# Kernel tuning notes

Hardware: AMD Instinct MI355X
Metric: run time of the kernel (lower is better)

The kernel has to match this reference:

```python
import jax, jax.numpy as jnp
import numpy as np

RADIUS = 0.3
NSAMPLE = 16
NPOINT = 256
EPS = 1e-5


def setup_inputs() -> dict:
    key = jax.random.key(0)
    ks = jax.random.split(key, 12)
    B, N, C = 16, 16384, 288
    d = {
        "xyz": jax.random.uniform(ks[0], (B, N, 3), jnp.float32),
        "features": jax.random.normal(ks[1], (B, C, N), jnp.float32),
    }
    cin = [C + 3, C, C]  # use_xyz adds 3 to first SharedMLP width
    for i in range(3):
        d[f"W{i}"] = jax.random.normal(ks[2 + i], (C, cin[i]), jnp.float32) / np.float32(np.sqrt(cin[i]))
        d[f"g{i}"] = jnp.ones((C,), jnp.float32)
        d[f"b{i}"] = jnp.zeros((C,), jnp.float32)
        d[f"m{i}"] = jax.random.normal(ks[5 + i], (C,), jnp.float32) * 0.1
        d[f"v{i}"] = jax.random.uniform(ks[8 + i], (C,), jnp.float32, minval=0.5, maxval=1.5)
    return d


def fps(xyz, npoint):
    """Farthest point sampling. xyz: (B,N,3) -> inds (B,npoint) int32."""
    B, N, _ = xyz.shape
    d0 = jnp.full((B, N), 1e10, xyz.dtype)
    i0 = jnp.zeros((B,), jnp.int32)  # CUDA kernel starts from index 0

    def step(carry, _):
        dist, idx = carry
        cur = jnp.take_along_axis(xyz, idx[:, None, None], axis=1)  # (B,1,3)
        d = jnp.sum((xyz - cur) ** 2, axis=-1)  # (B,N)
        dist = jnp.minimum(dist, d)
        nxt = jnp.argmax(dist, axis=-1).astype(jnp.int32)
        return (dist, nxt), idx

    _, inds = jax.lax.scan(step, (d0, i0), None, length=npoint)
    return inds.T  # (B, npoint)


def ball_query(xyz, new_xyz):
    """xyz: (B,N,3), new_xyz: (B,S,3) -> idx (B,S,NSAMPLE) int32.
    First NSAMPLE in-radius indices; pad with the first found index (CUDA semantics)."""
    N = xyz.shape[1]
    d2 = jnp.sum((new_xyz[:, :, None, :] - xyz[:, None, :, :]) ** 2, axis=-1)  # (B,S,N)
    mask = d2 < RADIUS * RADIUS
    cand = jnp.where(mask, jnp.arange(N, dtype=jnp.int32), jnp.int32(N))
    cand = jnp.sort(cand, axis=-1)[..., :NSAMPLE]
    first = cand[..., :1]
    return jnp.where(cand == N, first, cand)


def _mlp_bn_relu(h, W, g, b, m, v):
    # 1x1 Conv2d (no bias) + BatchNorm (running stats) + ReLU on (B,C,S,K)
    h = jnp.einsum('oc,bcsk->bosk', W, h)
    scale = (g * jax.lax.rsqrt(v + EPS))[:, None, None]
    return jax.nn.relu((h - m[:, None, None]) * scale + b[:, None, None])


def reference(xyz, features, W0, g0, b0, m0, v0, W1, g1, b1, m1, v1, W2, g2, b2, m2, v2):
    inds = fps(xyz, NPOINT)                                   # (B,S)
    new_xyz = jax.vmap(lambda p, i: p[i])(xyz, inds)          # (B,S,3)
    idx = ball_query(xyz, new_xyz)                            # (B,S,K)
    g_xyz = jax.vmap(lambda p, i: p[i])(xyz, idx)             # (B,S,K,3)
    g_xyz = (g_xyz - new_xyz[:, :, None, :]) / RADIUS         # normalize_xyz
    g_feat = jax.vmap(lambda f, i: f[:, i])(features, idx)    # (B,C,S,K)
    h = jnp.concatenate([jnp.transpose(g_xyz, (0, 3, 1, 2)), g_feat], axis=1)  # (B,C+3,S,K)
    for (W, g, b, m, v) in ((W0, g0, b0, m0, v0), (W1, g1, b1, m1, v1), (W2, g2, b2, m2, v2)):
        h = _mlp_bn_relu(h, W, g, b, m, v)
    new_features = jnp.max(h, axis=-1)                        # (B,C,S) max-pool over nsample
    return new_xyz, new_features, inds
```

## Files before the change

kernel.cpp:

```cpp
#include <hip/hip_runtime.h>
#include <hip/hip_bf16.h>
#include <string.h>

#define NPT   16384
#define NBAT  16
#define CH    288
#define SP    256
#define KS    16
#define OFF_FEAT 12288L
#define OFF_IND  1191936L

__device__ __forceinline__ float bfbits(unsigned short u){
  unsigned int x = ((unsigned int)u) << 16; float f; __builtin_memcpy(&f,&x,4); return f;
}
__device__ __forceinline__ float ldf(const void* p, long i, int isb){
  if (isb) return __bfloat162float(((const __hip_bfloat16*)p)[i]);
  return ((const float*)p)[i];
}
__device__ __forceinline__ void sto(void* p, long i, float v, int isb){
  if (isb) ((__hip_bfloat16*)p)[i] = __float2bfloat16(v);
  else     ((float*)p)[i] = v;
}
__device__ __forceinline__ void gload_lds(const void* g, void* l){
  __builtin_amdgcn_global_load_lds((const __attribute__((address_space(1))) void*)g,
      (__attribute__((address_space(3))) void*)l, 16, 0, 0);
}

typedef __attribute__((ext_vector_type(8))) short bf16x8;
typedef __attribute__((ext_vector_type(4))) float f32x4;

__global__ void detect_k(const void* __restrict__ xyz, int* __restrict__ flag){
  __shared__ float red[256];
  const int t = threadIdx.x;
  const unsigned short* u = (const unsigned short*)xyz;
  float m = 0.f;
  for (int i = t; i < 4096; i += 256){
    float f = fabsf(bfbits(u[i]));
    if (f != f) f = 1e30f;
    m = fmaxf(m, f);
  }
  red[t] = m; __syncthreads();
  for (int s = 128; s; s >>= 1){ if (t < s) red[t] = fmaxf(red[t], red[t+s]); __syncthreads(); }
  if (t == 0) *flag = (red[0] < 2.0f) ? 1 : 0;
}

__global__ __launch_bounds__(256) void cvtxyz_k(const void* __restrict__ xyz,
    const int* __restrict__ flag, float* __restrict__ X, float* __restrict__ Y,
    float* __restrict__ Z){
  const int e = blockIdx.x*256 + threadIdx.x;
  const int isb = *flag;
  float v = ldf(xyz, e, isb);
  int b = e / (NPT*3), r = e - b*(NPT*3), i = r/3, c = r - i*3;
  float* P = (c==0) ? X : ((c==1) ? Y : Z);
  P[b*NPT + i] = v;
}

__global__ __launch_bounds__(256) void cvtw_k(const void* __restrict__ W,
    const void* __restrict__ g, const void* __restrict__ bb,
    const void* __restrict__ m, const void* __restrict__ v,
    const int* __restrict__ flag, __hip_bfloat16* __restrict__ Wbf,
    float* __restrict__ scale, float* __restrict__ shift, int Kin){
  const int isb = *flag;
  const int idx = blockIdx.x*256 + threadIdx.x;
  if (idx < 288*296){
    int o = idx / 296, k = idx - o*296;
    float val = (k < Kin) ? ldf(W, (long)o*Kin + k, isb) : 0.f;
    Wbf[idx] = __float2bfloat16(val);
  }
  if (idx < 288){
    float sc = ldf(g, idx, isb) * rsqrtf(ldf(v, idx, isb) + 1e-5f);
    scale[idx] = sc;
    shift[idx] = ldf(bb, idx, isb) - ldf(m, idx, isb)*sc;
  }
}

__global__ __launch_bounds__(1024) __attribute__((amdgpu_waves_per_eu(4,4)))
void fps_k(const float* __restrict__ X,
    const float* __restrict__ Y, const float* __restrict__ Z,
    const int* __restrict__ flag, float* __restrict__ nxyz, void* __restrict__ dout){
  #pragma clang fp contract(off)
  const int b = blockIdx.x, t = threadIdx.x;
  const int base = b*NPT;
  float px[16], py[16], pz[16], dist[16];
  #pragma unroll
  for (int i=0;i<16;i++){
    px[i] = X[base + t + i*1024];
    py[i] = Y[base + t + i*1024];
    pz[i] = Z[base + t + i*1024];
    dist[i] = 1e10f;
  }
  __shared__ unsigned long long rk[2][16];
  __shared__ float ox[SP], oy[SP], oz[SP];
  __shared__ int   oi[SP];
  const int lane = t & 63, wid = t >> 6;
  const unsigned int lbase = 16383u - (unsigned int)t;
  float cx = X[base], cy = Y[base], cz = Z[base];
  int cur = 0;
  for (int it=0; it<SP; it++){
    if (t == 0){ ox[it]=cx; oy[it]=cy; oz[it]=cz; oi[it]=cur; }
    unsigned long long best = 0ull;
    #pragma unroll
    for (int i=0;i<16;i++){
      float dx = px[i]-cx, dy = py[i]-cy, dz = pz[i]-cz;
      float d2 = dx*dx + dy*dy; d2 = d2 + dz*dz;
      float dn = fminf(dist[i], d2); dist[i] = dn;
      unsigned long long key = ((unsigned long long)__float_as_uint(dn) << 32)
                             | (unsigned long long)(lbase - (unsigned int)(i*1024));
      best = (key > best) ? key : best;
    }
    #pragma unroll
    for (int off=32; off; off>>=1){
      unsigned long long o = __shfl_down(best, off, 64);
      best = (o > best) ? o : best;
    }
    const int p = it & 1;
    if (lane == 0) rk[p][wid] = best;
    __syncthreads();
    unsigned long long g0 = rk[p][0], g1 = rk[p][1], g2 = rk[p][2], g3 = rk[p][3];
    #pragma unroll
    for (int w=4; w<16; w+=4){
      unsigned long long a0=rk[p][w], a1=rk[p][w+1], a2=rk[p][w+2], a3=rk[p][w+3];
      g0=(a0>g0)?a0:g0; g1=(a1>g1)?a1:g1; g2=(a2>g2)?a2:g2; g3=(a3>g3)?a3:g3;
    }
    g0=(g1>g0)?g1:g0; g2=(g3>g2)?g3:g2; g0=(g2>g0)?g2:g0;
    cur = 16383 - (int)(unsigned int)g0;
    cx = X[base+cur]; cy = Y[base+cur]; cz = Z[base+cur];
  }
  __syncthreads();
  if (t < SP){
    const int isb = *flag;
    const long bs = (long)b*SP + t;
    float fx=ox[t], fy=oy[t], fz=oz[t]; int ii=oi[t];
    nxyz[bs*3+0]=fx; nxyz[bs*3+1]=fy; nxyz[bs*3+2]=fz;
    sto(dout, bs*3+0, fx, isb);
    sto(dout, bs*3+1, fy, isb);
    sto(dout, bs*3+2, fz, isb);
    sto(dout, OFF_IND + bs, (float)ii, isb);
  }
}

__global__ __launch_bounds__(256) void ballq_k(const float* __restrict__ X,
    const float* __restrict__ Y, const float* __restrict__ Z,
    const float* __restrict__ nxyz, int* __restrict__ bidx){
  #pragma clang fp contract(off)
  const int gw = (blockIdx.x*256 + threadIdx.x) >> 6;
  const int lane = threadIdx.x & 63;
  const int b = gw >> 8, base = b*NPT;
  const float cx = nxyz[gw*3+0], cy = nxyz[gw*3+1], cz = nxyz[gw*3+2];
  int cnt = 0, first = 0; bool havef = false;
  for (int st = 0; st < NPT && cnt < KS; st += 64){
    const int id = st + lane;
    float dx = X[base+id]-cx, dy = Y[base+id]-cy, dz = Z[base+id]-cz;
    float d2 = dx*dx + dy*dy; d2 = d2 + dz*dz;
    unsigned long long mk = __ballot(d2 <= 0.09f);
    if (mk){
      if (!havef){ first = st + __builtin_ctzll(mk); havef = true; }
      int rank = cnt + __popcll(mk & ((1ull<<lane)-1ull));
      if (((mk>>lane)&1ull) && rank < KS) bidx[gw*KS + rank] = id;
      cnt += __popcll(mk);
    }
  }
  if (cnt < KS && lane >= cnt && lane < KS) bidx[gw*KS + lane] = first;
}

__global__ __launch_bounds__(256) void gather_k(const void* __restrict__ xyz,
    const void* __restrict__ feat, const int* __restrict__ flag,
    const int* __restrict__ bidx, const float* __restrict__ nxyz,
    __hip_bfloat16* __restrict__ h0){
  __shared__ __hip_bfloat16 tile[64*296];
  const int isb = *flag;
  const int t = threadIdx.x, n0 = blockIdx.x*64;
  const int nl = t >> 2, cg = t & 3;
  const int n = n0 + nl, b = n >> 12, s = n >> 4;
  const int id = bidx[n];
  for (int j=0; j<74; j++){
    int c = cg*74 + j;
    float vv = 0.f;
    if (c < 3)       vv = (ldf(xyz, ((long)b*NPT + id)*3 + c, isb) - nxyz[(long)s*3 + c]) / 0.3f;
    else if (c < 291) vv = ldf(feat, ((long)b*CH + (c-3))*(long)NPT + id, isb);
    tile[nl*296 + c] = __float2bfloat16(vv);
  }
  __syncthreads();
  const uint4* src = (const uint4*)tile;
  uint4* dst = (uint4*)((char*)h0 + (long)n0*592);
  for (int j = t; j < 2368; j += 256) dst[j] = src[j];
}

__global__ __launch_bounds__(256, 2) void gemm_k(
    const __hip_bfloat16* __restrict__ A, int astr,
    const __hip_bfloat16* __restrict__ W,
    const float* __restrict__ scale, const float* __restrict__ shift,
    __hip_bfloat16* __restrict__ Out, int ostr,
    int ktiles, int kvalid){
  extern __shared__ char lds[];
  const int t = threadIdx.x, lane = t & 63, wid = t >> 6;
  const int wm = wid & 1, wo = wid >> 1;
  const int bx = blockIdx.x, by = blockIdx.y;
  {
    const char* src = (const char*)(A + (long)bx*128*astr);
    const int chunks = (128*astr*2) >> 10;
    for (int c = wid; c < chunks; c += 4)
      gload_lds(src + c*1024 + lane*16, lds + c*1024);
  }
  f32x4 acc[4][3];
  #pragma unroll
  for (int mf=0; mf<4; mf++)
    #pragma unroll
    for (int of=0; of<3; of++) acc[mf][of] = (f32x4){0.f,0.f,0.f,0.f};

  const int mrow  = wm*64 + (lane & 15);
  const int kg    = (lane >> 4) * 8;
  const int obase = by*96 + wo*48 + (lane & 15);
  __syncthreads();

  for (int kt = 0; kt < ktiles; kt++){
    const int k0 = kt*32 + kg;
    const bool z = (k0 >= kvalid);
    const int k0c = z ? 0 : k0;
    bf16x8 a[4], bf[3];
    #pragma unroll
    for (int mf=0; mf<4; mf++)
      a[mf] = *(const bf16x8*)(lds + ((long)(mrow + mf*16)*astr + k0c)*2);
    if (z){
      bf16x8 zz = {0,0,0,0,0,0,0,0};
      #pragma unroll
      for (int mf=0; mf<4; mf++) a[mf] = zz;
    }
    #pragma unroll
    for (int of=0; of<3; of++)
      bf[of] = *(const bf16x8*)(W + (long)(obase + of*16)*296 + k0c);
    #pragma unroll
    for (int mf=0; mf<4; mf++)
      #pragma unroll
      for (int of=0; of<3; of++)
        acc[mf][of] = __builtin_amdgcn_mfma_f32_16x16x32_bf16(a[mf], bf[of], acc[mf][of], 0, 0, 0);
  }

  float sc[3], sh[3];
  #pragma unroll
  for (int of=0; of<3; of++){ sc[of] = scale[obase + of*16]; sh[of] = shift[obase + of*16]; }
  #pragma unroll
  for (int mf=0; mf<4; mf++)
    #pragma unroll
    for (int of=0; of<3; of++)
      #pragma unroll
      for (int r=0; r<4; r++){
        const long row = (long)bx*128 + wm*64 + mf*16 + (lane>>4)*4 + r;
        const int o = obase + of*16;
        float vv = acc[mf][of][r]*sc[of] + sh[of];
        Out[row*ostr + o] = __float2bfloat16(fmaxf(vv, 0.f));
      }
}

__global__ __launch_bounds__(256) void maxk_k(const __hip_bfloat16* __restrict__ h,
    const int* __restrict__ flag, void* __restrict__ dout){
  __shared__ __hip_bfloat16 tile[128*288];
  const int isb = *flag;
  const int t = threadIdx.x;
  const int b = blockIdx.x >> 5, s0 = (blockIdx.x & 31)*8;
  const long n0 = (long)b*4096 + (long)s0*16;
  {
    const char* src = (const char*)(h + n0*288);
    for (int c = (t>>6); c < 72; c += 4)
      gload_lds(src + c*1024 + (t&63)*16, (char*)tile + c*1024);
  }
  __syncthreads();
  for (int o = t; o < 288; o += 256){
    float mx[8];
    #pragma unroll
    for (int sl=0; sl<8; sl++){
      float m = -1e30f;
      #pragma unroll
      for (int kk=0; kk<16; kk++)
        m = fmaxf(m, __bfloat162float(tile[(sl*16 + kk)*288 + o]));
      mx[sl] = m;
    }
    const long e0 = OFF_FEAT + (long)b*73728 + (long)o*256 + s0;
    if (isb){
      unsigned short u[8];
      #pragma unroll
      for (int sl=0; sl<8; sl++){
        __hip_bfloat16 hb = __float2bfloat16(mx[sl]);
        __builtin_memcpy(&u[sl], &hb, 2);
      }
      uint4 pk; __builtin_memcpy(&pk, u, 16);
      *(uint4*)((__hip_bfloat16*)dout + e0) = pk;
    } else {
      float* fo = (float*)dout + e0;
      *(float4*)fo     = make_float4(mx[0],mx[1],mx[2],mx[3]);
      *(float4*)(fo+4) = make_float4(mx[4],mx[5],mx[6],mx[7]);
    }
  }
}

extern "C" void kernel_launch(void* const* d_in, const int* in_sizes, int n_in,
                              void* d_out, int out_size, void* d_ws, size_t ws_size,
                              hipStream_t stream){
  const void* xyz  = d_in[0];
  const void* feat = d_in[1];
  const void* W0 = d_in[2];  const void* g0 = d_in[3];  const void* b0 = d_in[4];
  const void* m0 = d_in[5];  const void* v0 = d_in[6];
  const void* W1 = d_in[7];  const void* g1 = d_in[8];  const void* b1 = d_in[9];
  const void* m1 = d_in[10]; const void* v1 = d_in[11];
  const void* W2 = d_in[12]; const void* g2 = d_in[13]; const void* b2 = d_in[14];
  const void* m2 = d_in[15]; const void* v2 = d_in[16];

  char* ws = (char*)d_ws;
  int*   flag  = (int*)ws;
  float* sc0   = (float*)(ws + 64);
  float* sh0   = sc0 + 288;
  float* sc1   = sc0 + 576;  float* sh1 = sc0 + 864;
  float* sc2   = sc0 + 1152; float* sh2 = sc0 + 1440;
  __hip_bfloat16* Wb0 = (__hip_bfloat16*)(ws + 7040);
  __hip_bfloat16* Wb1 = Wb0 + 288*296;
  __hip_bfloat16* Wb2 = Wb1 + 288*296;
  float* nxyz = (float*)(ws + 518656);
  int*   bidx = (int*)(ws + 567808);
  float* X    = (float*)(ws + 1048576);
  float* Y    = X + NBAT*NPT;
  float* Z    = Y + NBAT*NPT;
  __hip_bfloat16* bufA = (__hip_bfloat16*)(ws + 1048576);
  __hip_bfloat16* bufB = (__hip_bfloat16*)(ws + 1048576 + 38797312);

  detect_k<<<1, 256, 0, stream>>>(xyz, flag);
  cvtxyz_k<<<3072, 256, 0, stream>>>(xyz, flag, X, Y, Z);
  cvtw_k<<<333, 256, 0, stream>>>(W0, g0, b0, m0, v0, flag, Wb0, sc0, sh0, 291);
  cvtw_k<<<333, 256, 0, stream>>>(W1, g1, b1, m1, v1, flag, Wb1, sc1, sh1, 288);
  cvtw_k<<<333, 256, 0, stream>>>(W2, g2, b2, m2, v2, flag, Wb2, sc2, sh2, 288);
  fps_k<<<NBAT, 1024, 0, stream>>>(X, Y, Z, flag, nxyz, d_out);
  ballq_k<<<1024, 256, 0, stream>>>(X, Y, Z, nxyz, bidx);
  gather_k<<<1024, 256, 0, stream>>>(xyz, feat, flag, bidx, nxyz, bufA);
  gemm_k<<<dim3(512,3), 256, 128*296*2, stream>>>(bufA, 296, Wb0, sc0, sh0, bufB, 288, 10, 296);
  gemm_k<<<dim3(512,3), 256, 128*288*2, stream>>>(bufB, 288, Wb1, sc1, sh1, bufA, 296, 9, 288);
  gemm_k<<<dim3(512,3), 256, 128*296*2, stream>>>(bufA, 296, Wb2, sc2, sh2, bufB, 288, 9, 288);
  maxk_k<<<512, 256, 0, stream>>>(bufB, flag, d_out);
}
```

Before: 1.061 ms.

## Morton-sort points per batch and skip FPS updates via per-wave bounding boxes

A new kernel bins each batch's points into a 16^3 Morton grid and counting-sorts them, keeping the original indices, so every wavefront in FPS owns a spatially compact cluster. FPS computes per-wave bounding boxes and skips the distance update and key reduction when the box's lower-bound distance to the new centroid exceeds the wave's current max min-distance. The final reduction uses shuffles and readfirstlane. This adds a sort pass and reuses the bufB workspace before the GEMMs; ties and near-equal cases depend on the 0.9999 safety margin.

```diff
diff --git a/kernel.cpp b/kernel.cpp
--- a/kernel.cpp
+++ b/kernel.cpp
@@ -24,6 +24,9 @@
 __device__ __forceinline__ void gload_lds(const void* g, void* l){
   __builtin_amdgcn_global_load_lds((const __attribute__((address_space(1))) void*)g,
       (__attribute__((address_space(3))) void*)l, 16, 0, 0);
+}
+__device__ __forceinline__ unsigned spread4(unsigned x){
+  return (x&1u) | ((x&2u)<<2) | ((x&4u)<<4) | ((x&8u)<<6);
 }
 
 typedef __attribute__((ext_vector_type(8))) short bf16x8;
@@ -74,56 +77,132 @@
   }
 }
 
+__global__ __launch_bounds__(1024) void sort_k(const float* __restrict__ X,
+    const float* __restrict__ Y, const float* __restrict__ Z,
+    float* __restrict__ X2, float* __restrict__ Y2, float* __restrict__ Z2,
+    int* __restrict__ I2){
+  __shared__ int hist[4096];
+  __shared__ int wtot[16];
+  const int b = blockIdx.x, t = threadIdx.x, base = b*NPT;
+  for (int j = t; j < 4096; j += 1024) hist[j] = 0;
+  __syncthreads();
+  int cell[16]; float lx[16], ly[16], lz[16];
+  #pragma unroll
+  for (int i=0;i<16;i++){
+    const int id = t + i*1024;
+    float x = X[base+id], y = Y[base+id], z = Z[base+id];
+    lx[i]=x; ly[i]=y; lz[i]=z;
+    int cx = (int)(x*16.f); cx = cx<0?0:(cx>15?15:cx);
+    int cy = (int)(y*16.f); cy = cy<0?0:(cy>15?15:cy);
+    int cz = (int)(z*16.f); cz = cz<0?0:(cz>15?15:cz);
+    cell[i] = (int)(spread4((unsigned)cx) | (spread4((unsigned)cy)<<1) | (spread4((unsigned)cz)<<2));
+    atomicAdd(&hist[cell[i]], 1);
+  }
+  __syncthreads();
+  int s0 = hist[t*4], s1 = hist[t*4+1], s2 = hist[t*4+2], s3 = hist[t*4+3];
+  int ls = s0+s1+s2+s3;
+  int sc = ls;
+  #pragma unroll
+  for (int off=1; off<64; off<<=1){
+    int o = __shfl_up(sc, off, 64);
+    if ((t&63) >= off) sc += o;
+  }
+  if ((t&63) == 63) wtot[t>>6] = sc;
+  __syncthreads();
+  int wpre = 0;
+  #pragma unroll
+  for (int w=0; w<16; w++) wpre += (w < (t>>6)) ? wtot[w] : 0;
+  const int ebase = wpre + sc - ls;
+  hist[t*4]   = ebase;
+  hist[t*4+1] = ebase + s0;
+  hist[t*4+2] = ebase + s0 + s1;
+  hist[t*4+3] = ebase + s0 + s1 + s2;
+  __syncthreads();
+  #pragma unroll
+  for (int i=0;i<16;i++){
+    const int dst = atomicAdd(&hist[cell[i]], 1);
+    X2[base+dst] = lx[i]; Y2[base+dst] = ly[i]; Z2[base+dst] = lz[i];
+    I2[base+dst] = t + i*1024;
+  }
+}
+
 __global__ __launch_bounds__(1024) __attribute__((amdgpu_waves_per_eu(4,4)))
-void fps_k(const float* __restrict__ X,
-    const float* __restrict__ Y, const float* __restrict__ Z,
+void fps_k(const float* __restrict__ X, const float* __restrict__ Y,
+    const float* __restrict__ Z,
+    const float* __restrict__ X2, const float* __restrict__ Y2,
+    const float* __restrict__ Z2, const int* __restrict__ I2,
     const int* __restrict__ flag, float* __restrict__ nxyz, void* __restrict__ dout){
   #pragma clang fp contract(off)
   const int b = blockIdx.x, t = threadIdx.x;
   const int base = b*NPT;
+  const int lane = t & 63, wid = t >> 6;
   float px[16], py[16], pz[16], dist[16];
+  unsigned int li[16];
+  const int p0 = base + wid*1024 + lane;
   #pragma unroll
   for (int i=0;i<16;i++){
-    px[i] = X[base + t + i*1024];
-    py[i] = Y[base + t + i*1024];
-    pz[i] = Z[base + t + i*1024];
+    px[i] = X2[p0 + i*64];
+    py[i] = Y2[p0 + i*64];
+    pz[i] = Z2[p0 + i*64];
+    li[i] = 16383u - (unsigned)I2[p0 + i*64];
     dist[i] = 1e10f;
   }
-  __shared__ unsigned long long rk[2][16];
+  float bxn=px[0],bxx=px[0],byn=py[0],byx=py[0],bzn=pz[0],bzx=pz[0];
+  #pragma unroll
+  for (int i=1;i<16;i++){
+    bxn=fminf(bxn,px[i]); bxx=fmaxf(bxx,px[i]);
+    byn=fminf(byn,py[i]); byx=fmaxf(byx,py[i]);
+    bzn=fminf(bzn,pz[i]); bzx=fmaxf(bzx,pz[i]);
+  }
+  #pragma unroll
+  for (int off=32; off; off>>=1){
+    bxn=fminf(bxn,__shfl_xor(bxn,off,64)); bxx=fmaxf(bxx,__shfl_xor(bxx,off,64));
+    byn=fminf(byn,__shfl_xor(byn,off,64)); byx=fmaxf(byx,__shfl_xor(byx,off,64));
+    bzn=fminf(bzn,__shfl_xor(bzn,off,64)); bzx=fmaxf(bzx,__shfl_xor(bzx,off,64));
+  }
+  __shared__ unsigned long long slot[2][16];
   __shared__ float ox[SP], oy[SP], oz[SP];
   __shared__ int   oi[SP];
-  const int lane = t & 63, wid = t >> 6;
-  const unsigned int lbase = 16383u - (unsigned int)t;
   float cx = X[base], cy = Y[base], cz = Z[base];
   int cur = 0;
+  unsigned long long wkey = 0ull;
+  float wavemax = 1e30f;
   for (int it=0; it<SP; it++){
     if (t == 0){ ox[it]=cx; oy[it]=cy; oz[it]=cz; oi[it]=cur; }
-    unsigned long long best = 0ull;
-    #pragma unroll
-    for (int i=0;i<16;i++){
-      float dx = px[i]-cx, dy = py[i]-cy, dz = pz[i]-cz;
-      float d2 = dx*dx + dy*dy; d2 = d2 + dz*dz;
-      float dn = fminf(dist[i], d2); dist[i] = dn;
-      unsigned long long key = ((unsigned long long)__float_as_uint(dn) << 32)
-                             | (unsigned long long)(lbase - (unsigned int)(i*1024));
-      best = (key > best) ? key : best;
-    }
-    #pragma unroll
-    for (int off=32; off; off>>=1){
-      unsigned long long o = __shfl_down(best, off, 64);
-      best = (o > best) ? o : best;
+    float ddx = fmaxf(fmaxf(bxn-cx, cx-bxx), 0.f);
+    float ddy = fmaxf(fmaxf(byn-cy, cy-byx), 0.f);
+    float ddz = fmaxf(fmaxf(bzn-cz, cz-bzx), 0.f);
+    float lb = ddx*ddx + ddy*ddy + ddz*ddz;
+    if (!(lb * 0.9999f > wavemax)){
+      unsigned long long best = 0ull;
+      #pragma unroll
+      for (int i=0;i<16;i++){
+        float dx = px[i]-cx, dy = py[i]-cy, dz = pz[i]-cz;
+        float d2 = dx*dx + dy*dy; d2 = d2 + dz*dz;
+        float dn = fminf(dist[i], d2); dist[i] = dn;
+        unsigned long long key = ((unsigned long long)__float_as_uint(dn) << 32)
+                               | (unsigned long long)li[i];
+        best = (key > best) ? key : best;
+      }
+      #pragma unroll
+      for (int off=32; off; off>>=1){
+        unsigned long long o = __shfl_xor(best, off, 64);
+        best = (o > best) ? o : best;
+      }
+      wkey = best;
+      wavemax = __uint_as_float((unsigned)(best >> 32));
     }
     const int p = it & 1;
-    if (lane == 0) rk[p][wid] = best;
+    if (lane == 0) slot[p][wid] = wkey;
     __syncthreads();
-    unsigned long long g0 = rk[p][0], g1 = rk[p][1], g2 = rk[p][2], g3 = rk[p][3];
-    #pragma unroll
-    for (int w=4; w<16; w+=4){
-      unsigned long long a0=rk[p][w], a1=rk[p][w+1], a2=rk[p][w+2], a3=rk[p][w+3];
-      g0=(a0>g0)?a0:g0; g1=(a1>g1)?a1:g1; g2=(a2>g2)?a2:g2; g3=(a3>g3)?a3:g3;
-    }
-    g0=(g1>g0)?g1:g0; g2=(g3>g2)?g3:g2; g0=(g2>g0)?g2:g0;
-    cur = 16383 - (int)(unsigned int)g0;
+    unsigned long long g = slot[p][lane & 15];
+    #pragma unroll
+    for (int m=8; m; m>>=1){
+      unsigned long long o = __shfl_xor(g, m, 64);
+      g = (o > g) ? o : g;
+    }
+    cur = 16383 - (int)(unsigned)g;
+    cur = __builtin_amdgcn_readfirstlane(cur);
     cx = X[base+cur]; cy = Y[base+cur]; cz = Z[base+cur];
   }
   __syncthreads();
@@ -321,13 +400,18 @@
   float* Z    = Y + NBAT*NPT;
   __hip_bfloat16* bufA = (__hip_bfloat16*)(ws + 1048576);
   __hip_bfloat16* bufB = (__hip_bfloat16*)(ws + 1048576 + 38797312);
+  float* X2 = (float*)bufB;
+  float* Y2 = X2 + NBAT*NPT;
+  float* Z2 = Y2 + NBAT*NPT;
+  int*   I2 = (int*)(Z2 + NBAT*NPT);
 
   detect_k<<<1, 256, 0, stream>>>(xyz, flag);
   cvtxyz_k<<<3072, 256, 0, stream>>>(xyz, flag, X, Y, Z);
   cvtw_k<<<333, 256, 0, stream>>>(W0, g0, b0, m0, v0, flag, Wb0, sc0, sh0, 291);
   cvtw_k<<<333, 256, 0, stream>>>(W1, g1, b1, m1, v1, flag, Wb1, sc1, sh1, 288);
   cvtw_k<<<333, 256, 0, stream>>>(W2, g2, b2, m2, v2, flag, Wb2, sc2, sh2, 288);
-  fps_k<<<NBAT, 1024, 0, stream>>>(X, Y, Z, flag, nxyz, d_out);
+  sort_k<<<NBAT, 1024, 0, stream>>>(X, Y, Z, X2, Y2, Z2, I2);
+  fps_k<<<NBAT, 1024, 0, stream>>>(X, Y, Z, X2, Y2, Z2, I2, flag, nxyz, d_out);
   ballq_k<<<1024, 256, 0, stream>>>(X, Y, Z, nxyz, bidx);
   gather_k<<<1024, 256, 0, stream>>>(xyz, feat, flag, bidx, nxyz, bufA);
   gemm_k<<<dim3(512,3), 256, 128*296*2, stream>>>(bufA, 296, Wb0, sc0, sh0, bufB, 288, 10, 296);
```

After: 1.012 ms. -4.6%, faster.
